# Performance work log

Hardware: AMD Instinct MI355X
Metric: run time of the kernel (lower is better)

Reference implementation:

```python
import jax, jax.numpy as jnp
import numpy as np

TOP_K = 2  # matches init kwarg top_k


def setup_inputs() -> dict:
    key = jax.random.key(0)
    k1, k2, k3 = jax.random.split(key, 3)
    N, D, H, E = 8192, 2048, 2048, 8
    x = jax.random.normal(k1, (N, D), dtype=jnp.float32)
    Wg = jax.random.normal(k2, (D, E), dtype=jnp.float32) * (1.0 / np.sqrt(D))
    bg = jnp.zeros((E,), dtype=jnp.float32)
    We = jax.random.normal(k3, (E, D, H), dtype=jnp.float32) * (1.0 / np.sqrt(D))
    be = jnp.zeros((E, H), dtype=jnp.float32)
    return {"x": x, "Wg": Wg, "bg": bg, "We": We, "be": be}


def reference(x, Wg, bg, We, be):
    # Gating: softmax over experts, then keep only top-k weights per token.
    gate = jax.nn.softmax(x @ Wg + bg, axis=-1)          # [N, E]
    top_v, top_i = jax.lax.top_k(gate, TOP_K)            # [N, K]
    E = gate.shape[-1]
    # Sparse combine weights: zeros except top-k entries (weights NOT renormalized,
    # matching the original which uses raw softmax scores).
    comb = jnp.sum(jax.nn.one_hot(top_i, E, dtype=gate.dtype) * top_v[..., None], axis=1)  # [N, E]
    # Per-expert linear applied to every token (dense dispatch), then weighted sum.
    expert_out = jnp.einsum('nd,edh->neh', x, We) + be   # [N, E, H]
    out = jnp.einsum('ne,neh->nh', comb, expert_out)     # [N, H]
    return out
```

## Files before the change

### kernel.cpp

```cpp
#include <hip/hip_runtime.h>

#define N_TOK 8192
#define DIM   2048
#define HID   2048
#define NE    8
#define BK    128
#define NKT   (DIM / BK)

typedef unsigned short u16;
typedef __attribute__((ext_vector_type(4))) float f4v;
typedef __attribute__((ext_vector_type(8))) short s8v;

__device__ __forceinline__ unsigned int cvtpk(float lo, float hi) {
  unsigned int r;
  asm volatile("v_cvt_pk_bf16_f32 %0, %1, %2" : "=v"(r) : "v"(lo), "v"(hi));
  return r;
}

__global__ __launch_bounds__(256) void gating_kernel(
    const float* __restrict__ x, const float* __restrict__ Wg,
    const float* __restrict__ bg, int* __restrict__ sel,
    float* __restrict__ wslot)
{
  __shared__ float wg_lds[NE][DIM];
  #pragma unroll
  for (int i = 0; i < 16; ++i) {
    int f = threadIdx.x + 256 * i;
    int d = f >> 1, ep = (f & 1) * 4;
    float4 w = reinterpret_cast<const float4*>(Wg)[f];
    wg_lds[ep + 0][d] = w.x; wg_lds[ep + 1][d] = w.y;
    wg_lds[ep + 2][d] = w.z; wg_lds[ep + 3][d] = w.w;
  }
  __syncthreads();

  int wave = threadIdx.x >> 6, lane = threadIdx.x & 63;
  #pragma unroll 2
  for (int j = 0; j < 4; ++j) {
    int n = blockIdx.x * 16 + wave * 4 + j;
    const float4* x4 = reinterpret_cast<const float4*>(x + (size_t)n * DIM);
    float acc[NE] = {0.f,0.f,0.f,0.f,0.f,0.f,0.f,0.f};
    #pragma unroll
    for (int i = 0; i < 8; ++i) {
      int d4 = lane + 64 * i;
      float4 xv = x4[d4];
      #pragma unroll
      for (int e = 0; e < NE; ++e) {
        float4 w = *reinterpret_cast<const float4*>(&wg_lds[e][d4 * 4]);
        acc[e] += xv.x * w.x + xv.y * w.y + xv.z * w.z + xv.w * w.w;
      }
    }
    #pragma unroll
    for (int e = 0; e < NE; ++e)
      #pragma unroll
      for (int off = 32; off; off >>= 1)
        acc[e] += __shfl_xor(acc[e], off);

    if (lane == 0) {
      float m = -1e30f;
      #pragma unroll
      for (int e = 0; e < NE; ++e) { acc[e] += bg[e]; m = fmaxf(m, acc[e]); }
      float p[NE]; float s = 0.f;
      #pragma unroll
      for (int e = 0; e < NE; ++e) { p[e] = expf(acc[e] - m); s += p[e]; }
      float inv = 1.0f / s;
      int e1 = 0; float v1 = p[0];
      #pragma unroll
      for (int e = 1; e < NE; ++e) if (p[e] > v1) { v1 = p[e]; e1 = e; }
      int e2 = -1; float v2 = -1.f;
      #pragma unroll
      for (int e = 0; e < NE; ++e) if (e != e1 && p[e] > v2) { v2 = p[e]; e2 = e; }
      sel[n] = e1 | (e2 << 4);
      wslot[n] = v1 * inv;
      wslot[N_TOK + n] = v2 * inv;
    }
  }
}

__global__ __launch_bounds__(256) void build_lists_kernel(
    const int* __restrict__ sel, int* __restrict__ counts, int* __restrict__ lists)
{
  __shared__ int wsum[4];
  __shared__ int runbase;
  int b = blockIdx.x;
  int s = b >> 3, e = b & 7;
  int t = threadIdx.x, lane = t & 63, wave = t >> 6;
  if (t == 0) runbase = 0;
  __syncthreads();
  int* listp = lists + (size_t)b * N_TOK;
  for (int base = 0; base < N_TOK; base += 256) {
    int n = base + t;
    int sv = sel[n];
    int field = s ? (sv >> 4) : (sv & 15);
    bool p = (field == e);
    unsigned long long mask = __ballot(p);
    int rank = __popcll(mask & ((1ull << lane) - 1ull));
    int wtot = __popcll(mask);
    if (lane == 0) wsum[wave] = wtot;
    __syncthreads();
    int wbase = 0;
    #pragma unroll
    for (int w = 0; w < 4; ++w) wbase += (w < wave) ? wsum[w] : 0;
    int tot = wsum[0] + wsum[1] + wsum[2] + wsum[3];
    if (p) listp[runbase + wbase + rank] = n;
    __syncthreads();
    if (t == 0) runbase += tot;
    __syncthreads();
  }
  if (t == 0) counts[b] = runbase;
}

__global__ void build_desc_kernel(const int* __restrict__ counts,
                                  int* __restrict__ gfirst, int* __restrict__ desc)
{
  if (threadIdx.x == 0 && blockIdx.x == 0) {
    for (int s = 0; s < 2; ++s) {
      int tc = 0;
      for (int e = 0; e < NE; ++e) {
        gfirst[s * 9 + e] = tc;
        int nt = (counts[s * NE + e] + 127) >> 7;
        for (int i = 0; i < nt; ++i) desc[s * 71 + tc++] = (e << 8) | i;
      }
      gfirst[s * 9 + 8] = tc;
    }
  }
}

template <int PHASE>
__global__ __launch_bounds__(512) void moe_gemm_f32(
    const float* __restrict__ xf, const float* __restrict__ Wef,
    const float* __restrict__ be, const int* __restrict__ counts,
    const int* __restrict__ gfirst, const int* __restrict__ desc,
    const int* __restrict__ lists, const float* __restrict__ wslot,
    float* __restrict__ out)
{
  __shared__ __align__(16) u16 A_lds[128 * BK];
  __shared__ __align__(16) u16 B_lds[128 * BK];
  __shared__ int   tok_lds[128];
  __shared__ float wgt_lds[128];

  const int ntile = blockIdx.x;
  const int idx   = blockIdx.y;
  if (idx >= gfirst[PHASE * 9 + 8]) return;
  const int d  = desc[PHASE * 71 + idx];
  const int e  = d >> 8;
  const int mt = d & 255;
  const int cnt = counts[PHASE * NE + e];

  const int t = threadIdx.x;
  if (t < 128) {
    int r = mt * 128 + t;
    int rc = (r < cnt) ? r : (cnt - 1);
    int tok = lists[(PHASE * NE + e) * N_TOK + rc];
    tok_lds[t] = tok;
    wgt_lds[t] = wslot[PHASE * N_TOK + tok];
  }
  __syncthreads();

  const int lane = t & 63, wid = t >> 6;
  const int wm = (wid & 3) * 32, wn = (wid >> 2) * 64;
  const int lrow = lane & 15, lkg = lane >> 4;

  f4v acc[2][4];
  f4v zero = {0.f, 0.f, 0.f, 0.f};
  #pragma unroll
  for (int mi = 0; mi < 2; ++mi)
    #pragma unroll
    for (int ni = 0; ni < 4; ++ni) acc[mi][ni] = zero;

  const float* wef = Wef + (size_t)e * DIM * HID;

  const float* ap[8]; unsigned int ab[8];
  #pragma unroll
  for (int i = 0; i < 8; ++i) {
    int flat = t + 512 * i;
    int row = flat >> 5, c4 = flat & 31;
    ap[i] = xf + (size_t)tok_lds[row] * DIM + c4 * 4;
    ab[i] = (unsigned int)(row * 256)
          + ((((unsigned int)(c4 >> 1) ^ ((unsigned int)row & 15u)) << 4)
             | (((unsigned int)c4 & 1u) << 3));
  }
  const int bn = t & 127, bh = t >> 7;
  const float* bp0 = wef + (size_t)(bh * 32) * HID + ntile * 128 + bn;
  unsigned int bbyte[4];
  #pragma unroll
  for (int q = 0; q < 4; ++q)
    bbyte[q] = (unsigned int)(bn * 256)
             + (((unsigned int)(bh * 4 + q) ^ ((unsigned int)bn & 15u)) << 4);

  #pragma unroll 1
  for (int kt = 0; kt < NKT; ++kt) {
    float4 av[8];
    #pragma unroll
    for (int i = 0; i < 8; ++i)
      av[i] = *reinterpret_cast<const float4*>(ap[i] + kt * BK);
    float bv[32];
    const float* bpk = bp0 + (size_t)kt * BK * HID;
    #pragma unroll
    for (int j = 0; j < 32; ++j)
      bv[j] = bpk[(size_t)j * HID];

    #pragma unroll
    for (int i = 0; i < 8; ++i) {
      uint2 w; w.x = cvtpk(av[i].x, av[i].y); w.y = cvtpk(av[i].z, av[i].w);
      *reinterpret_cast<uint2*>(reinterpret_cast<char*>(A_lds) + ab[i]) = w;
    }
    #pragma unroll
    for (int q = 0; q < 4; ++q) {
      union { unsigned int w[4]; s8v v; } ub;
      ub.w[0] = cvtpk(bv[q * 8 + 0], bv[q * 8 + 1]);
      ub.w[1] = cvtpk(bv[q * 8 + 2], bv[q * 8 + 3]);
      ub.w[2] = cvtpk(bv[q * 8 + 4], bv[q * 8 + 5]);
      ub.w[3] = cvtpk(bv[q * 8 + 6], bv[q * 8 + 7]);
      *reinterpret_cast<s8v*>(reinterpret_cast<char*>(B_lds) + bbyte[q]) = ub.v;
    }
    __syncthreads();
    #pragma unroll
    for (int kk = 0; kk < 4; ++kk) {
      unsigned int unit = (unsigned int)(kk * 4 + lkg);
      s8v a[2], b[4];
      #pragma unroll
      for (int i = 0; i < 2; ++i) {
        unsigned int arow = (unsigned int)(wm + i * 16 + lrow);
        a[i] = *reinterpret_cast<const s8v*>(reinterpret_cast<const char*>(A_lds)
               + arow * 256u + ((unit ^ (arow & 15u)) << 4));
      }
      #pragma unroll
      for (int i = 0; i < 4; ++i) {
        unsigned int brow = (unsigned int)(wn + i * 16 + lrow);
        b[i] = *reinterpret_cast<const s8v*>(reinterpret_cast<const char*>(B_lds)
               + brow * 256u + ((unit ^ (brow & 15u)) << 4));
      }
      #pragma unroll
      for (int mi = 0; mi < 2; ++mi)
        #pragma unroll
        for (int ni = 0; ni < 4; ++ni)
          acc[mi][ni] = __builtin_amdgcn_mfma_f32_16x16x32_bf16(a[mi], b[ni], acc[mi][ni], 0, 0, 0);
    }
    __syncthreads();
  }

  const float* bev = be + (size_t)e * HID + ntile * 128;
  #pragma unroll
  for (int ni = 0; ni < 4; ++ni) {
    int col = wn + ni * 16 + lrow;
    float bevv = bev[col];
    #pragma unroll
    for (int mi = 0; mi < 2; ++mi) {
      #pragma unroll
      for (int q = 0; q < 4; ++q) {
        int row = wm + mi * 16 + lkg * 4 + q;
        if (mt * 128 + row < cnt) {
          int tok = tok_lds[row];
          float w = wgt_lds[row];
          float v = w * (acc[mi][ni][q] + bevv);
          float* o = out + (size_t)tok * HID + ntile * 128 + col;
          if (PHASE == 0) *o = v; else *o += v;
        }
      }
    }
  }
}

extern "C" void kernel_launch(void* const* d_in, const int* in_sizes, int n_in,
                              void* d_out, int out_size, void* d_ws, size_t ws_size,
                              hipStream_t stream) {
  const float* x  = (const float*)d_in[0];
  const float* Wg = (const float*)d_in[1];
  const float* bg = (const float*)d_in[2];
  const float* We = (const float*)d_in[3];
  const float* be = (const float*)d_in[4];
  float* out = (float*)d_out;
  char* ws = (char*)d_ws;

  int*   counts = (int*)ws;
  int*   gfirst = (int*)(ws + 64);
  int*   desc   = (int*)(ws + 256);
  int*   sel    = (int*)(ws + 1024);
  float* wslot  = (float*)(ws + 33792);
  int*   lists  = (int*)(ws + 99328);

  hipLaunchKernelGGL(gating_kernel, dim3(512), dim3(256), 0, stream,
                     x, Wg, bg, sel, wslot);
  hipLaunchKernelGGL(build_lists_kernel, dim3(16), dim3(256), 0, stream,
                     sel, counts, lists);
  hipLaunchKernelGGL(build_desc_kernel, dim3(1), dim3(64), 0, stream,
                     counts, gfirst, desc);

  dim3 ggrid(16, 71);
  hipLaunchKernelGGL((moe_gemm_f32<0>), ggrid, dim3(512), 0, stream,
                     x, We, be, counts, gfirst, desc, lists, wslot, out);
  hipLaunchKernelGGL((moe_gemm_f32<1>), ggrid, dim3(512), 0, stream,
                     x, We, be, counts, gfirst, desc, lists, wslot, out);
}
```

Before: 531.9 us.

## Enlarge GEMM tiles to 256x256 with BK 64 and 8x4 MFMA per wave

Changes the expert GEMM block tile from 128x128 with BK=128 to 256x256 with BK=64. Each wave now computes a 128x64 sub-tile with 32 accumulators, and the LDS layout and swizzle are reworked to match. The bigger tile raises arithmetic intensity and reduces how often each block reloads the fp32 x and We data through global memory. In exchange it adds register pressure from the 128 accumulator floats per lane, halves the number of row tiles per expert (grid shrinks to 8x39), and produces more padded rows on partially filled tiles.

```diff
diff --git a/kernel.cpp b/kernel.cpp
--- a/kernel.cpp
+++ b/kernel.cpp
@@ -4,7 +4,7 @@
 #define DIM   2048
 #define HID   2048
 #define NE    8
-#define BK    128
+#define BK    64
 #define NKT   (DIM / BK)
 
 typedef unsigned short u16;
@@ -117,7 +117,7 @@
       int tc = 0;
       for (int e = 0; e < NE; ++e) {
         gfirst[s * 9 + e] = tc;
-        int nt = (counts[s * NE + e] + 127) >> 7;
+        int nt = (counts[s * NE + e] + 255) >> 8;
         for (int i = 0; i < nt; ++i) desc[s * 71 + tc++] = (e << 8) | i;
       }
       gfirst[s * 9 + 8] = tc;
@@ -133,10 +133,10 @@
     const int* __restrict__ lists, const float* __restrict__ wslot,
     float* __restrict__ out)
 {
-  __shared__ __align__(16) u16 A_lds[128 * BK];
-  __shared__ __align__(16) u16 B_lds[128 * BK];
-  __shared__ int   tok_lds[128];
-  __shared__ float wgt_lds[128];
+  __shared__ __align__(16) u16 A_lds[256 * BK];
+  __shared__ __align__(16) u16 B_lds[256 * BK];
+  __shared__ int   tok_lds[256];
+  __shared__ float wgt_lds[256];
 
   const int ntile = blockIdx.x;
   const int idx   = blockIdx.y;
@@ -147,8 +147,8 @@
   const int cnt = counts[PHASE * NE + e];
 
   const int t = threadIdx.x;
-  if (t < 128) {
-    int r = mt * 128 + t;
+  if (t < 256) {
+    int r = mt * 256 + t;
     int rc = (r < cnt) ? r : (cnt - 1);
     int tok = lists[(PHASE * NE + e) * N_TOK + rc];
     tok_lds[t] = tok;
@@ -157,42 +157,39 @@
   __syncthreads();
 
   const int lane = t & 63, wid = t >> 6;
-  const int wm = (wid & 3) * 32, wn = (wid >> 2) * 64;
+  const int wm = (wid & 1) * 128, wn = (wid >> 1) * 64;
   const int lrow = lane & 15, lkg = lane >> 4;
 
-  f4v acc[2][4];
+  f4v acc[8][4];
   f4v zero = {0.f, 0.f, 0.f, 0.f};
   #pragma unroll
-  for (int mi = 0; mi < 2; ++mi)
+  for (int mi = 0; mi < 8; ++mi)
     #pragma unroll
     for (int ni = 0; ni < 4; ++ni) acc[mi][ni] = zero;
 
   const float* wef = Wef + (size_t)e * DIM * HID;
 
-  const float* ap[8]; unsigned int ab[8];
+  unsigned int aoff[8]; unsigned int ab[8];
   #pragma unroll
   for (int i = 0; i < 8; ++i) {
     int flat = t + 512 * i;
-    int row = flat >> 5, c4 = flat & 31;
-    ap[i] = xf + (size_t)tok_lds[row] * DIM + c4 * 4;
-    ab[i] = (unsigned int)(row * 256)
-          + ((((unsigned int)(c4 >> 1) ^ ((unsigned int)row & 15u)) << 4)
-             | (((unsigned int)c4 & 1u) << 3));
-  }
-  const int bn = t & 127, bh = t >> 7;
-  const float* bp0 = wef + (size_t)(bh * 32) * HID + ntile * 128 + bn;
-  unsigned int bbyte[4];
-  #pragma unroll
-  for (int q = 0; q < 4; ++q)
-    bbyte[q] = (unsigned int)(bn * 256)
-             + (((unsigned int)(bh * 4 + q) ^ ((unsigned int)bn & 15u)) << 4);
+    int row = flat >> 4, c4 = flat & 15;
+    aoff[i] = (unsigned int)(tok_lds[row] * DIM + c4 * 4);
+    ab[i] = ((unsigned int)(row * 128 + c4 * 8)) ^ (((unsigned int)row & 7u) << 4);
+  }
+  const int bn = t & 255, bh = t >> 8;
+  const float* bp0 = wef + (size_t)(bh * 32) * HID + ntile * 256 + bn;
+  unsigned int bbyte[8];
+  #pragma unroll
+  for (int kb = 0; kb < 8; ++kb)
+    bbyte[kb] = ((unsigned int)(bn * 128 + bh * 64 + kb * 8)) ^ (((unsigned int)bn & 7u) << 4);
 
   #pragma unroll 1
   for (int kt = 0; kt < NKT; ++kt) {
     float4 av[8];
     #pragma unroll
     for (int i = 0; i < 8; ++i)
-      av[i] = *reinterpret_cast<const float4*>(ap[i] + kt * BK);
+      av[i] = *reinterpret_cast<const float4*>(xf + aoff[i] + kt * BK);
     float bv[32];
     const float* bpk = bp0 + (size_t)kt * BK * HID;
     #pragma unroll
@@ -205,55 +202,50 @@
       *reinterpret_cast<uint2*>(reinterpret_cast<char*>(A_lds) + ab[i]) = w;
     }
     #pragma unroll
-    for (int q = 0; q < 4; ++q) {
-      union { unsigned int w[4]; s8v v; } ub;
-      ub.w[0] = cvtpk(bv[q * 8 + 0], bv[q * 8 + 1]);
-      ub.w[1] = cvtpk(bv[q * 8 + 2], bv[q * 8 + 3]);
-      ub.w[2] = cvtpk(bv[q * 8 + 4], bv[q * 8 + 5]);
-      ub.w[3] = cvtpk(bv[q * 8 + 6], bv[q * 8 + 7]);
-      *reinterpret_cast<s8v*>(reinterpret_cast<char*>(B_lds) + bbyte[q]) = ub.v;
-    }
-    __syncthreads();
-    #pragma unroll
-    for (int kk = 0; kk < 4; ++kk) {
-      unsigned int unit = (unsigned int)(kk * 4 + lkg);
-      s8v a[2], b[4];
-      #pragma unroll
-      for (int i = 0; i < 2; ++i) {
-        unsigned int arow = (unsigned int)(wm + i * 16 + lrow);
-        a[i] = *reinterpret_cast<const s8v*>(reinterpret_cast<const char*>(A_lds)
-               + arow * 256u + ((unit ^ (arow & 15u)) << 4));
-      }
-      #pragma unroll
-      for (int i = 0; i < 4; ++i) {
-        unsigned int brow = (unsigned int)(wn + i * 16 + lrow);
-        b[i] = *reinterpret_cast<const s8v*>(reinterpret_cast<const char*>(B_lds)
-               + brow * 256u + ((unit ^ (brow & 15u)) << 4));
-      }
-      #pragma unroll
-      for (int mi = 0; mi < 2; ++mi)
+    for (int kb = 0; kb < 8; ++kb) {
+      uint2 w; w.x = cvtpk(bv[kb * 4 + 0], bv[kb * 4 + 1]);
+               w.y = cvtpk(bv[kb * 4 + 2], bv[kb * 4 + 3]);
+      *reinterpret_cast<uint2*>(reinterpret_cast<char*>(B_lds) + bbyte[kb]) = w;
+    }
+    __syncthreads();
+    #pragma unroll
+    for (int kk2 = 0; kk2 < 2; ++kk2) {
+      unsigned int koff = (unsigned int)(kk2 * 64 + lkg * 16);
+      s8v b[4];
+      #pragma unroll
+      for (int ni = 0; ni < 4; ++ni) {
+        unsigned int brow = (unsigned int)(wn + ni * 16 + lrow);
+        b[ni] = *reinterpret_cast<const s8v*>(
+            reinterpret_cast<const char*>(B_lds) + ((brow * 128u + koff) ^ ((brow & 7u) << 4)));
+      }
+      #pragma unroll
+      for (int mi = 0; mi < 8; ++mi) {
+        unsigned int arow = (unsigned int)(wm + mi * 16 + lrow);
+        s8v a = *reinterpret_cast<const s8v*>(
+            reinterpret_cast<const char*>(A_lds) + ((arow * 128u + koff) ^ ((arow & 7u) << 4)));
         #pragma unroll
         for (int ni = 0; ni < 4; ++ni)
-          acc[mi][ni] = __builtin_amdgcn_mfma_f32_16x16x32_bf16(a[mi], b[ni], acc[mi][ni], 0, 0, 0);
-    }
-    __syncthreads();
-  }
-
-  const float* bev = be + (size_t)e * HID + ntile * 128;
+          acc[mi][ni] = __builtin_amdgcn_mfma_f32_16x16x32_bf16(a, b[ni], acc[mi][ni], 0, 0, 0);
+      }
+    }
+    __syncthreads();
+  }
+
+  const float* bev = be + (size_t)e * HID + ntile * 256;
   #pragma unroll
   for (int ni = 0; ni < 4; ++ni) {
     int col = wn + ni * 16 + lrow;
     float bevv = bev[col];
     #pragma unroll
-    for (int mi = 0; mi < 2; ++mi) {
+    for (int mi = 0; mi < 8; ++mi) {
       #pragma unroll
       for (int q = 0; q < 4; ++q) {
         int row = wm + mi * 16 + lkg * 4 + q;
-        if (mt * 128 + row < cnt) {
+        if (mt * 256 + row < cnt) {
           int tok = tok_lds[row];
           float w = wgt_lds[row];
           float v = w * (acc[mi][ni][q] + bevv);
-          float* o = out + (size_t)tok * HID + ntile * 128 + col;
+          float* o = out + (size_t)tok * HID + ntile * 256 + col;
           if (PHASE == 0) *o = v; else *o += v;
         }
       }
@@ -286,7 +278,7 @@
   hipLaunchKernelGGL(build_desc_kernel, dim3(1), dim3(64), 0, stream,
                      counts, gfirst, desc);
 
-  dim3 ggrid(16, 71);
+  dim3 ggrid(HID / 256, 39);
   hipLaunchKernelGGL((moe_gemm_f32<0>), ggrid, dim3(512), 0, stream,
                      x, We, be, counts, gfirst, desc, lists, wslot, out);
   hipLaunchKernelGGL((moe_gemm_f32<1>), ggrid, dim3(512), 0, stream,
```

Result: slower. 552.3 us (+3.8%).
